# Kernel tuning notes

Measured on AMD Instinct MI355X. Metric: run time of the kernel, lower is better.

Reference implementation:

```python
import jax, jax.numpy as jnp
import numpy as np

B, T, D = 2, 128, 1024
H, R, Dk, Dv = 8, 8, 64, 64


def setup_inputs() -> dict:
    key = jax.random.key(0)
    ks = jax.random.split(key, 11)
    w = lambda k, shp: jax.random.normal(k, shp, dtype=jnp.float32) * 0.02
    return {
        "hidden_states": jax.random.normal(ks[0], (B, T, D), dtype=jnp.float32),
        "Wq": w(ks[1], (D, H * Dk)),
        "Wk": w(ks[2], (D, H * Dk)),
        "Wv": w(ks[3], (D, H * Dv)),
        "Wb": w(ks[4], (D, H * R)),
        "Wtg": w(ks[5], (D, H * R)),
        "mode_logits": jax.random.normal(ks[6], (H, R), dtype=jnp.float32) * 0.1,
        "log_decay": jax.random.normal(ks[7], (H, R), dtype=jnp.float32) * 0.1,
        "omega_log_scale": jax.random.normal(ks[8], (H, R), dtype=jnp.float32) * 0.1,
        "Wg": w(ks[9], (D, H * Dv)),
        "Wo": w(ks[10], (H * Dv, D)),
    }


def _forward(x, Wq, Wk, Wv, Wb, Wtg, mode_logits, log_decay, omega_log_scale, Wg, Wo):
    b, t, _ = x.shape
    # projections
    q = (x @ Wq).reshape(b, t, H, Dk)
    k = (x @ Wk).reshape(b, t, H, Dk)
    v = (x @ Wv).reshape(b, t, H, Dv)
    beta = jax.nn.sigmoid((x @ Wb).reshape(b, t, H, R))
    tg = jax.nn.sigmoid((x @ Wtg).reshape(b, t, H, R))
    # spectral mode parameters
    pair_idx = jnp.arange(0, Dk, 2, dtype=jnp.float32)
    inv_freq = 1.0 / (10000.0 ** (pair_idx / Dk))            # [Dk/2]
    omega = jnp.exp(omega_log_scale)[..., None] * inv_freq    # [H,R,Dk/2]
    omega_full = jnp.repeat(omega, 2, axis=-1)                # [H,R,Dk] (repeat_interleave)
    cos_w = jnp.cos(omega_full)[None, :, :, None, :]          # [1,H,R,1,Dk]
    sin_w = jnp.sin(omega_full)[None, :, :, None, :]
    rho = jnp.exp(-jax.nn.softplus(log_decay))                # [H,R]
    mode_w = jax.nn.softmax(mode_logits, axis=-1)             # [H,R]

    # time-major for scan
    qT = jnp.moveaxis(q, 1, 0)
    kT = jnp.moveaxis(k, 1, 0)
    vT = jnp.moveaxis(v, 1, 0)
    betaT = jnp.moveaxis(beta, 1, 0)
    tgT = jnp.moveaxis(tg, 1, 0)

    def step(carry, xs):
        sr, si = carry                      # [B,H,R,Dv,Dk] each
        q_t, k_t, v_t, b_t, g_t = xs
        decay = (g_t * rho)[..., None, None]            # [B,H,R,1,1]
        rot_r = decay * (cos_w * sr - sin_w * si)
        rot_i = decay * (sin_w * sr + cos_w * si)
        pred = jnp.einsum('bhrvk,bhk->bhrv', rot_r, k_t)
        err = v_t[:, :, None, :] - pred                  # [B,H,R,Dv]
        write = err[..., None] * k_t[:, :, None, None, :]
        sr_new = rot_r + b_t[..., None, None] * write
        read = jnp.einsum('bhrvk,bhk->bhrv', sr_new, q_t)
        y = jnp.einsum('bhrv,hr->bhv', read, mode_w)     # [B,H,Dv]
        return (sr_new, rot_i), y

    s0 = jnp.zeros((b, H, R, Dv, Dk), dtype=x.dtype)
    _, ys = jax.lax.scan(step, (s0, s0), (qT, kT, vT, betaT, tgT))
    o = jnp.moveaxis(ys, 0, 1)                           # [B,T,H,Dv]
    gate = jax.nn.sigmoid((x @ Wg).reshape(b, t, H, Dv))
    o = (o * gate).reshape(b, t, H * Dv)
    return o @ Wo


def reference(hidden_states, Wq, Wk, Wv, Wb, Wtg, mode_logits, log_decay,
              omega_log_scale, Wg, Wo):
    return _forward(hidden_states, Wq, Wk, Wv, Wb, Wtg, mode_logits,
                    log_decay, omega_log_scale, Wg, Wo)
```

## Files before the change

kernel.cpp:

```cpp
#include <hip/hip_runtime.h>
#include <math.h>

#define T_ 128
#define NPROJ 2176
#define CH 32

typedef __attribute__((ext_vector_type(8))) short short8;
typedef __attribute__((ext_vector_type(4))) float float4v;
typedef __attribute__((ext_vector_type(2))) float float2v;

__device__ __forceinline__ ushort f2bf(float x) {
    unsigned u = __float_as_uint(x);
    u += 0x7FFF + ((u >> 16) & 1);
    return (ushort)(u >> 16);
}
__device__ __forceinline__ unsigned pack_bf(float a, float b) {
    unsigned ua = (__float_as_uint(a) + 0x8000u) >> 16;
    unsigned ub = (__float_as_uint(b) + 0x8000u) & 0xffff0000u;
    return ua | ub;
}
__device__ __forceinline__ float bf_lo(unsigned w) { return __uint_as_float(w << 16); }
__device__ __forceinline__ float bf_hi(unsigned w) { return __uint_as_float(w & 0xffff0000u); }

template<int CTRL>
__device__ __forceinline__ float dpp_add(float x) {
    int xi = __float_as_int(x);
    int yi = __builtin_amdgcn_update_dpp(xi, xi, CTRL, 0xF, 0xF, false);
    return x + __int_as_float(yi);
}

__global__ __launch_bounds__(256) void prep_kernel(
    const float* __restrict__ x,
    const float* __restrict__ Wq, const float* __restrict__ Wk,
    const float* __restrict__ Wv, const float* __restrict__ Wb,
    const float* __restrict__ Wtg, const float* __restrict__ Wg,
    const float* __restrict__ Wo,
    const float* __restrict__ mode_logits, const float* __restrict__ log_decay,
    const float* __restrict__ ols,
    float* __restrict__ cosw, float* __restrict__ sinw,
    float* __restrict__ rho, float* __restrict__ modew,
    ushort* __restrict__ xb, ushort* __restrict__ wtb, ushort* __restrict__ wotb,
    float* __restrict__ Acomb)
{
    __shared__ ushort tile[64][68];
    const int blk = blockIdx.x, tid = threadIdx.x;
    if (blk < 16) {
        int idx = blk * 256 + tid;
        if (idx >= 64 * 64) return;
        int t = idx >> 6;
        int k = idx & 63;
        int h = t >> 3;
        if (k == 0) {
            float ld = log_decay[t];
            rho[t] = 1.0f / (1.0f + expf(ld));
            float m = -1e30f;
            for (int i = 0; i < 8; i++) m = fmaxf(m, mode_logits[h * 8 + i]);
            float sum = 0.0f;
            for (int i = 0; i < 8; i++) sum += expf(mode_logits[h * 8 + i] - m);
            modew[t] = expf(mode_logits[t] - m) / sum;
        }
        float osc = expf(ols[t]);
        int p = k >> 1;
        float invf = expf(-((float)(2 * p) / 64.0f) * logf(10000.0f));
        float w = osc * invf;
        cosw[idx] = cosf(w);
        sinw[idx] = sinf(w);
        return;
    }
    if (blk < 80) {
        int base = (blk - 16) * 4096 + tid * 16;
        float4 f0 = *(const float4*)&x[base];
        float4 f1 = *(const float4*)&x[base + 4];
        float4 f2 = *(const float4*)&x[base + 8];
        float4 f3 = *(const float4*)&x[base + 12];
        short8 o0, o1;
        o0[0]=f2bf(f0.x); o0[1]=f2bf(f0.y); o0[2]=f2bf(f0.z); o0[3]=f2bf(f0.w);
        o0[4]=f2bf(f1.x); o0[5]=f2bf(f1.y); o0[6]=f2bf(f1.z); o0[7]=f2bf(f1.w);
        o1[0]=f2bf(f2.x); o1[1]=f2bf(f2.y); o1[2]=f2bf(f2.z); o1[3]=f2bf(f2.w);
        o1[4]=f2bf(f3.x); o1[5]=f2bf(f3.y); o1[6]=f2bf(f3.z); o1[7]=f2bf(f3.w);
        *(short8*)&xb[base] = o0;
        *(short8*)&xb[base + 8] = o1;
        return;
    }
    if (blk >= 752) {
        int base = (blk - 752) * 4096 + tid * 16;
        float4 z = make_float4(0.f, 0.f, 0.f, 0.f);
        *(float4*)&Acomb[base] = z;
        *(float4*)&Acomb[base + 4] = z;
        *(float4*)&Acomb[base + 8] = z;
        *(float4*)&Acomb[base + 12] = z;
        return;
    }
    const float* src; int ld, c0, n0, k0, ldd; ushort* dst;
    if (blk < 624) {
        int b3 = blk - 80; int nt = b3 >> 4, kt = b3 & 15;
        n0 = nt * 64; k0 = kt * 64;
        if (n0 < 512)       { src = Wq;  c0 = n0;        ld = 512; }
        else if (n0 < 1024) { src = Wk;  c0 = n0 - 512;  ld = 512; }
        else if (n0 < 1536) { src = Wv;  c0 = n0 - 1024; ld = 512; }
        else if (n0 < 1600) { src = Wb;  c0 = n0 - 1536; ld = 64;  }
        else if (n0 < 1664) { src = Wtg; c0 = n0 - 1600; ld = 64;  }
        else                { src = Wg;  c0 = n0 - 1664; ld = 512; }
        dst = wtb; ldd = 1024;
    } else {
        int b4 = blk - 624; int nt = b4 >> 3, kt = b4 & 7;
        n0 = nt * 64; k0 = kt * 64;
        src = Wo; c0 = n0; ld = 1024; dst = wotb; ldd = 512;
    }
    #pragma unroll
    for (int rep = 0; rep < 4; rep++) {
        int k = rep * 16 + (tid >> 4);
        int nc = (tid & 15) * 4;
        float4 f = *(const float4*)&src[(size_t)(k0 + k) * ld + c0 + nc];
        tile[nc + 0][k] = f2bf(f.x);
        tile[nc + 1][k] = f2bf(f.y);
        tile[nc + 2][k] = f2bf(f.z);
        tile[nc + 3][k] = f2bf(f.w);
    }
    __syncthreads();
    #pragma unroll
    for (int rep = 0; rep < 4; rep++) {
        int n = rep * 16 + (tid >> 4);
        int kc = (tid & 15) * 4;
        uint2 uu = *(const uint2*)&tile[n][kc];
        *(uint2*)&dst[(size_t)(n0 + n) * ldd + k0 + kc] = uu;
    }
}

__global__ __launch_bounds__(256, 2) void proj_mfma(const ushort* __restrict__ Ab,
        const ushort* __restrict__ BTb, const float* __restrict__ rho,
        float* __restrict__ proj)
{
    __shared__ ushort sA[2][64][40];
    __shared__ ushort sB[2][64][40];
    const int n0 = blockIdx.x * 64, m0 = blockIdx.y * 64;
    const int tid = threadIdx.x;
    const int lane = tid & 63, w = tid >> 6;
    const int wm = w & 1, wn = w >> 1;
    const int l16 = lane & 15, quad = lane >> 4;
    const int srow = tid >> 2, skq = (tid & 3) * 8;
    const ushort* Ag = Ab + (size_t)(m0 + srow) * 1024 + skq;
    const ushort* Bg = BTb + (size_t)(n0 + srow) * 1024 + skq;
    short8 raA = *(const short8*)Ag;
    short8 rbA = *(const short8*)Bg;
    short8 raB = *(const short8*)(Ag + 32);
    short8 rbB = *(const short8*)(Bg + 32);
    float4v acc00 = {0,0,0,0}, acc01 = {0,0,0,0}, acc10 = {0,0,0,0}, acc11 = {0,0,0,0};
    for (int kt = 0; kt < 32; kt += 2) {
        *(short8*)&sA[0][srow][skq] = raA;
        *(short8*)&sB[0][srow][skq] = rbA;
        __syncthreads();
        if (kt + 2 < 32) {
            raA = *(const short8*)(Ag + (kt + 2) * 32);
            rbA = *(const short8*)(Bg + (kt + 2) * 32);
        }
        {
            short8 a0 = *(const short8*)&sA[0][wm * 32 + l16][quad * 8];
            short8 a1 = *(const short8*)&sA[0][wm * 32 + 16 + l16][quad * 8];
            short8 b0 = *(const short8*)&sB[0][wn * 32 + l16][quad * 8];
            short8 b1 = *(const short8*)&sB[0][wn * 32 + 16 + l16][quad * 8];
            acc00 = __builtin_amdgcn_mfma_f32_16x16x32_bf16(a0, b0, acc00, 0, 0, 0);
            acc01 = __builtin_amdgcn_mfma_f32_16x16x32_bf16(a0, b1, acc01, 0, 0, 0);
            acc10 = __builtin_amdgcn_mfma_f32_16x16x32_bf16(a1, b0, acc10, 0, 0, 0);
            acc11 = __builtin_amdgcn_mfma_f32_16x16x32_bf16(a1, b1, acc11, 0, 0, 0);
        }
        *(short8*)&sA[1][srow][skq] = raB;
        *(short8*)&sB[1][srow][skq] = rbB;
        __syncthreads();
        if (kt + 3 < 32) {
            raB = *(const short8*)(Ag + (kt + 3) * 32);
            rbB = *(const short8*)(Bg + (kt + 3) * 32);
        }
        {
            short8 a0 = *(const short8*)&sA[1][wm * 32 + l16][quad * 8];
            short8 a1 = *(const short8*)&sA[1][wm * 32 + 16 + l16][quad * 8];
            short8 b0 = *(const short8*)&sB[1][wn * 32 + l16][quad * 8];
            short8 b1 = *(const short8*)&sB[1][wn * 32 + 16 + l16][quad * 8];
            acc00 = __builtin_amdgcn_mfma_f32_16x16x32_bf16(a0, b0, acc00, 0, 0, 0);
            acc01 = __builtin_amdgcn_mfma_f32_16x16x32_bf16(a0, b1, acc01, 0, 0, 0);
            acc10 = __builtin_amdgcn_mfma_f32_16x16x32_bf16(a1, b0, acc10, 0, 0, 0);
            acc11 = __builtin_amdgcn_mfma_f32_16x16x32_bf16(a1, b1, acc11, 0, 0, 0);
        }
    }
    const bool sig = (n0 >= 1536);
    float m0c = 1.0f, m1c = 1.0f;
    if (n0 == 1600) {
        m0c = rho[wn * 32 + l16];
        m1c = rho[wn * 32 + l16 + 16];
    }
    const int colb = n0 + wn * 32 + l16;
    const int rowb = m0 + wm * 32 + quad * 4;
    #pragma unroll
    for (int r2 = 0; r2 < 4; r2++) {
        float v00 = acc00[r2], v01 = acc01[r2], v10 = acc10[r2], v11 = acc11[r2];
        if (sig) {
            v00 = m0c / (1.0f + expf(-v00));
            v01 = m1c / (1.0f + expf(-v01));
            v10 = m0c / (1.0f + expf(-v10));
            v11 = m1c / (1.0f + expf(-v11));
        }
        proj[(size_t)(rowb + r2) * NPROJ + colb] = v00;
        proj[(size_t)(rowb + r2) * NPROJ + colb + 16] = v01;
        proj[(size_t)(rowb + 16 + r2) * NPROJ + colb] = v10;
        proj[(size_t)(rowb + 16 + r2) * NPROJ + colb + 16] = v11;
    }
}

__global__ __launch_bounds__(256, 2) void scan_kernel(const float* __restrict__ proj,
        const float* __restrict__ cosw, const float* __restrict__ sinw,
        const float* __restrict__ modew, float* __restrict__ Acomb)
{
    __shared__ uint2 qks[2][CH][16][2];
    __shared__ float2 vg[2][CH][16];
    __shared__ float sc4[2][CH][4];
    __shared__ float obuf[CH][16];

    const int bi = blockIdx.x;
    const int s  = bi & 3;
    const int hr = (bi >> 2) & 63;
    const int b  = bi >> 8;
    const int h = hr >> 3, r = hr & 7;
    const int tid = threadIdx.x;
    const int vl = tid >> 4;
    const int kl = tid & 15;

    float2v cw0, cw1, sw0, sw1;
    cw0.x = cosw[hr * 64 + kl * 4 + 0]; cw0.y = cosw[hr * 64 + kl * 4 + 1];
    cw1.x = cosw[hr * 64 + kl * 4 + 2]; cw1.y = cosw[hr * 64 + kl * 4 + 3];
    sw0.x = sinw[hr * 64 + kl * 4 + 0]; sw0.y = sinw[hr * 64 + kl * 4 + 1];
    sw1.x = sinw[hr * 64 + kl * 4 + 2]; sw1.y = sinw[hr * 64 + kl * 4 + 3];
    const float mw = modew[hr];
    float2v sr0 = {0,0}, sr1 = {0,0}, si0 = {0,0}, si1 = {0,0};

    const float* pb = proj + (size_t)b * T_ * NPROJ;
    const int qbase = h * 64;
    const int kbase = 512 + h * 64;
    const int vbase = 1024 + h * 64 + s * 16;
    const int gbase = 1664 + h * 64 + s * 16;
    const int boff  = 1536 + h * 8 + r;
    const int goff  = 1600 + h * 8 + r;

    {
        #pragma unroll
        for (int rep = 0; rep < 4; rep++) {
            int idx = rep * 256 + tid;
            int t = idx >> 5, sub = idx & 31;
            const float* row = pb + (size_t)t * NPROJ;
            float4 f = *(const float4*)(row + (sub < 16 ? qbase + sub * 4
                                                        : kbase + (sub - 16) * 4));
            uint2 pk2; pk2.x = pack_bf(f.x, f.y); pk2.y = pack_bf(f.z, f.w);
            qks[0][t][sub & 15][sub < 16 ? 1 : 0] = pk2;
        }
        #pragma unroll
        for (int rep = 0; rep < 2; rep++) {
            int idx = rep * 256 + tid;
            int t = idx >> 4, v2 = idx & 15;
            const float* row = pb + (size_t)t * NPROJ;
            vg[0][t][v2] = make_float2(row[vbase + v2], row[gbase + v2]);
        }
        if (tid < CH)            sc4[0][tid][0]      = pb[(size_t)tid * NPROJ + boff];
        else if (tid < 2 * CH)   sc4[0][tid - CH][1] = pb[(size_t)(tid - CH) * NPROJ + goff];
    }
    __syncthreads();

    float* dstb = Acomb + ((size_t)b * 128) * 512 + h * 64 + s * 16;

    for (int c = 0; c < T_ / CH; c++) {
        const int cb = c & 1, nb = cb ^ 1;
        const bool have = (c + 1 < T_ / CH);

        float4 g_qk[4]; float2 g_vg[2]; float g_sc = 0.0f;
        if (have) {
            const int t0 = (c + 1) * CH;
            #pragma unroll
            for (int rep = 0; rep < 4; rep++) {
                int idx = rep * 256 + tid;
                int t = idx >> 5, sub = idx & 31;
                const float* row = pb + (size_t)(t0 + t) * NPROJ;
                g_qk[rep] = *(const float4*)(row + (sub < 16 ? qbase + sub * 4
                                                             : kbase + (sub - 16) * 4));
            }
            #pragma unroll
            for (int rep = 0; rep < 2; rep++) {
                int idx = rep * 256 + tid;
                int t = idx >> 4, v2 = idx & 15;
                const float* row = pb + (size_t)(t0 + t) * NPROJ;
                g_vg[rep] = make_float2(row[vbase + v2], row[gbase + v2]);
            }
            if (tid < CH)          g_sc = pb[(size_t)(t0 + tid) * NPROJ + boff];
            else if (tid < 2 * CH) g_sc = pb[(size_t)(t0 + tid - CH) * NPROJ + goff];
        }

        {
            int t = tid >> 3, j = tid & 7;
            uint4 wa = *(const uint4*)&qks[cb][t][2 * j][0];
            uint4 wb = *(const uint4*)&qks[cb][t][2 * j + 1][0];
            float p = bf_lo(wa.x) * bf_lo(wa.z) + bf_hi(wa.x) * bf_hi(wa.z)
                    + bf_lo(wa.y) * bf_lo(wa.w) + bf_hi(wa.y) * bf_hi(wa.w)
                    + bf_lo(wb.x) * bf_lo(wb.z) + bf_hi(wb.x) * bf_hi(wb.z)
                    + bf_lo(wb.y) * bf_lo(wb.w) + bf_hi(wb.y) * bf_hi(wb.w);
            p = dpp_add<0xB1>(p);
            p = dpp_add<0x4E>(p);
            p = dpp_add<0x141>(p);
            if (j == 0) sc4[cb][t][2] = p;
        }
        if (c > 0) {
            #pragma unroll
            for (int rep = 0; rep < 2; rep++) {
                int idx = rep * 256 + tid;
                int t = idx >> 4, v2 = idx & 15;
                atomicAdd(dstb + (size_t)((c - 1) * CH + t) * 512 + v2, obuf[t][v2]);
            }
        }
        __syncthreads();

        const float2* vgb = &vg[cb][0][0];
        const float4* svb = (const float4*)&sc4[cb][0][0];

        uint4 w = *(const uint4*)&qks[cb][0][kl][0];
        float4 sv = svb[0];
        float2 vgv = vgb[vl];
        #pragma unroll
        for (int t = 0; t < CH; t++) {
            uint4 w_n; float4 sv_n; float2 vg_n;
            if (t + 1 < CH) {
                w_n = *(const uint4*)&qks[cb][t + 1][kl][0];
                sv_n = svb[t + 1];
                vg_n = vgb[(t + 1) * 16 + vl];
            }

            float2v k0; k0.x = bf_lo(w.x); k0.y = bf_hi(w.x);
            float2v k1; k1.x = bf_lo(w.y); k1.y = bf_hi(w.y);
            float2v q0; q0.x = bf_lo(w.z); q0.y = bf_hi(w.z);
            float2v q1; q1.x = bf_lo(w.w); q1.y = bf_hi(w.w);

            const float decay = sv.y;
            float2v t1 = cw0 * sr0 - sw0 * si0;
            float2v u1 = sw0 * sr0 + cw0 * si0;
            float2v t2 = cw1 * sr1 - sw1 * si1;
            float2v u2 = sw1 * sr1 + cw1 * si1;
            float2v d2; d2.x = decay; d2.y = decay;
            float2v rr0 = d2 * t1, rr1 = d2 * t2;
            si0 = d2 * u1; si1 = d2 * u2;

            float2v pk2 = rr0 * k0 + rr1 * k1;
            float2v pq2 = rr0 * q0 + rr1 * q1;
            float pk = pk2.x + pk2.y;
            float pq = pq2.x + pq2.y;
            pk = dpp_add<0xB1>(pk);  pq = dpp_add<0xB1>(pq);
            pk = dpp_add<0x4E>(pk);  pq = dpp_add<0x4E>(pq);
            pk = dpp_add<0x141>(pk); pq = dpp_add<0x141>(pq);
            pk = dpp_add<0x140>(pk); pq = dpp_add<0x140>(pq);

            const float sc = sv.x * (vgv.x - pk);
            float2v sc2; sc2.x = sc; sc2.y = sc;
            sr0 = rr0 + sc2 * k0;
            sr1 = rr1 + sc2 * k1;
            const float rp = pq + sc * sv.z;
            if (kl == 0) obuf[t][vl] = mw * rp * vgv.y;

            w = w_n; sv = sv_n; vgv = vg_n;
        }

        if (have) {
            #pragma unroll
            for (int rep = 0; rep < 4; rep++) {
                int idx = rep * 256 + tid;
                int t = idx >> 5, sub = idx & 31;
                float4 f = g_qk[rep];
                uint2 pk2; pk2.x = pack_bf(f.x, f.y); pk2.y = pack_bf(f.z, f.w);
                qks[nb][t][sub & 15][sub < 16 ? 1 : 0] = pk2;
            }
            #pragma unroll
            for (int rep = 0; rep < 2; rep++) {
                int idx = rep * 256 + tid;
                int t = idx >> 4, v2 = idx & 15;
                vg[nb][t][v2] = g_vg[rep];
            }
            if (tid < CH)          sc4[nb][tid][0]      = g_sc;
            else if (tid < 2 * CH) sc4[nb][tid - CH][1] = g_sc;
        }
        __syncthreads();
    }
    #pragma unroll
    for (int rep = 0; rep < 2; rep++) {
        int idx = rep * 256 + tid;
        int t = idx >> 4, v2 = idx & 15;
        atomicAdd(dstb + (size_t)(3 * CH + t) * 512 + v2, obuf[t][v2]);
    }
}

__global__ __launch_bounds__(256, 2) void out_mfma(const float* __restrict__ Af,
        const ushort* __restrict__ BTb, float* __restrict__ C)
{
    __shared__ ushort sA[2][64][40];
    __shared__ ushort sB[2][64][40];
    const int n0 = blockIdx.x * 64, m0 = blockIdx.y * 64;
    const int tid = threadIdx.x;
    const int lane = tid & 63, w = tid >> 6;
    const int wm = w & 1, wn = w >> 1;
    const int l16 = lane & 15, quad = lane >> 4;
    const int srow = tid >> 2, skq = (tid & 3) * 8;
    const float* Ag = Af + (size_t)(m0 + srow) * 512 + skq;
    const ushort* Bg = BTb + (size_t)(n0 + srow) * 512 + skq;
    float4 fa0A = *(const float4*)Ag;
    float4 fa1A = *(const float4*)(Ag + 4);
    short8 rbA  = *(const short8*)Bg;
    float4 fa0B = *(const float4*)(Ag + 32);
    float4 fa1B = *(const float4*)(Ag + 36);
    short8 rbB  = *(const short8*)(Bg + 32);
    float4v acc00 = {0,0,0,0}, acc01 = {0,0,0,0}, acc10 = {0,0,0,0}, acc11 = {0,0,0,0};
    for (int kt = 0; kt < 16; kt += 2) {
        {
            short8 ra;
            ra[0]=f2bf(fa0A.x); ra[1]=f2bf(fa0A.y); ra[2]=f2bf(fa0A.z); ra[3]=f2bf(fa0A.w);
            ra[4]=f2bf(fa1A.x); ra[5]=f2bf(fa1A.y); ra[6]=f2bf(fa1A.z); ra[7]=f2bf(fa1A.w);
            *(short8*)&sA[0][srow][skq] = ra;
            *(short8*)&sB[0][srow][skq] = rbA;
        }
        __syncthreads();
        if (kt + 2 < 16) {
            fa0A = *(const float4*)(Ag + (kt + 2) * 32);
            fa1A = *(const float4*)(Ag + (kt + 2) * 32 + 4);
            rbA  = *(const short8*)(Bg + (kt + 2) * 32);
        }
        {
            short8 a0 = *(const short8*)&sA[0][wm * 32 + l16][quad * 8];
            short8 a1 = *(const short8*)&sA[0][wm * 32 + 16 + l16][quad * 8];
            short8 b0 = *(const short8*)&sB[0][wn * 32 + l16][quad * 8];
            short8 b1 = *(const short8*)&sB[0][wn * 32 + 16 + l16][quad * 8];
            acc00 = __builtin_amdgcn_mfma_f32_16x16x32_bf16(a0, b0, acc00, 0, 0, 0);
            acc01 = __builtin_amdgcn_mfma_f32_16x16x32_bf16(a0, b1, acc01, 0, 0, 0);
            acc10 = __builtin_amdgcn_mfma_f32_16x16x32_bf16(a1, b0, acc10, 0, 0, 0);
            acc11 = __builtin_amdgcn_mfma_f32_16x16x32_bf16(a1, b1, acc11, 0, 0, 0);
        }
        {
            short8 ra;
            ra[0]=f2bf(fa0B.x); ra[1]=f2bf(fa0B.y); ra[2]=f2bf(fa0B.z); ra[3]=f2bf(fa0B.w);
            ra[4]=f2bf(fa1B.x); ra[5]=f2bf(fa1B.y); ra[6]=f2bf(fa1B.z); ra[7]=f2bf(fa1B.w);
            *(short8*)&sA[1][srow][skq] = ra;
            *(short8*)&sB[1][srow][skq] = rbB;
        }
        __syncthreads();
        if (kt + 3 < 16) {
            fa0B = *(const float4*)(Ag + (kt + 3) * 32);
            fa1B = *(const float4*)(Ag + (kt + 3) * 32 + 4);
            rbB  = *(const short8*)(Bg + (kt + 3) * 32);
        }
        {
            short8 a0 = *(const short8*)&sA[1][wm * 32 + l16][quad * 8];
            short8 a1 = *(const short8*)&sA[1][wm * 32 + 16 + l16][quad * 8];
            short8 b0 = *(const short8*)&sB[1][wn * 32 + l16][quad * 8];
            short8 b1 = *(const short8*)&sB[1][wn * 32 + 16 + l16][quad * 8];
            acc00 = __builtin_amdgcn_mfma_f32_16x16x32_bf16(a0, b0, acc00, 0, 0, 0);
            acc01 = __builtin_amdgcn_mfma_f32_16x16x32_bf16(a0, b1, acc01, 0, 0, 0);
            acc10 = __builtin_amdgcn_mfma_f32_16x16x32_bf16(a1, b0, acc10, 0, 0, 0);
            acc11 = __builtin_amdgcn_mfma_f32_16x16x32_bf16(a1, b1, acc11, 0, 0, 0);
        }
    }
    const int colb = n0 + wn * 32 + l16;
    const int rowb = m0 + wm * 32 + quad * 4;
    #pragma unroll
    for (int r2 = 0; r2 < 4; r2++) {
        C[(size_t)(rowb + r2) * 1024 + colb] = acc00[r2];
        C[(size_t)(rowb + r2) * 1024 + colb + 16] = acc01[r2];
        C[(size_t)(rowb + 16 + r2) * 1024 + colb] = acc10[r2];
        C[(size_t)(rowb + 16 + r2) * 1024 + colb + 16] = acc11[r2];
    }
}

extern "C" void kernel_launch(void* const* d_in, const int* in_sizes, int n_in,
                              void* d_out, int out_size, void* d_ws, size_t ws_size,
                              hipStream_t stream) {
    const float* x   = (const float*)d_in[0];
    const float* Wq  = (const float*)d_in[1];
    const float* Wk  = (const float*)d_in[2];
    const float* Wv  = (const float*)d_in[3];
    const float* Wb  = (const float*)d_in[4];
    const float* Wtg = (const float*)d_in[5];
    const float* ml  = (const float*)d_in[6];
    const float* ldc = (const float*)d_in[7];
    const float* ols = (const float*)d_in[8];
    const float* Wg  = (const float*)d_in[9];
    const float* Wo  = (const float*)d_in[10];
    float* out = (float*)d_out;

    float* ws = (float*)d_ws;
    float* proj    = ws;
    float* cosw    = proj + 256 * NPROJ;
    float* sinw    = cosw + 4096;
    float* rho     = sinw + 4096;
    float* modew   = rho + 64;
    ushort* xb     = (ushort*)(modew + 64);
    ushort* wotb   = (ushort*)((float*)xb + 131072);
    float*  Acomb  = (float*)wotb + 262144;
    ushort* wtb    = (ushort*)(Acomb + 131072);

    prep_kernel<<<784, 256, 0, stream>>>(x, Wq, Wk, Wv, Wb, Wtg, Wg, Wo,
                                         ml, ldc, ols, cosw, sinw, rho, modew,
                                         xb, wtb, wotb, Acomb);
    proj_mfma<<<dim3(34, 4), 256, 0, stream>>>(xb, wtb, rho, proj);
    scan_kernel<<<512, 256, 0, stream>>>(proj, cosw, sinw, modew, Acomb);
    out_mfma<<<dim3(16, 4), 256, 0, stream>>>(Acomb, wotb, out);
}
```

Measured before the change: 135.1 us.

## Split scan state across 512 threads with two k-elements each

The scan kernel now launches 512 threads per block. Each thread holds 2 k-dimension elements of the state instead of 4, and the dot-product reductions gain a ds_swizzle step so they span 32 lanes. The decay multiply is moved out of the reduction chain and applied to the reduced scalars afterwards, which shortens the serial dependency inside each time step. The q/k shared-memory layout and the staging loads are reorganised to match. The aim is to cut per-step latency in the sequential recurrence, at the cost of an extra cross-lane shuffle, more threads per block and possible occupancy pressure.

```diff
diff --git a/kernel.cpp b/kernel.cpp
--- a/kernel.cpp
+++ b/kernel.cpp
@@ -26,6 +26,10 @@
 __device__ __forceinline__ float dpp_add(float x) {
     int xi = __float_as_int(x);
     int yi = __builtin_amdgcn_update_dpp(xi, xi, CTRL, 0xF, 0xF, false);
+    return x + __int_as_float(yi);
+}
+__device__ __forceinline__ float swz_add16(float x) {
+    int yi = __builtin_amdgcn_ds_swizzle(__float_as_int(x), 0x401F);
     return x + __int_as_float(yi);
 }
 
@@ -206,11 +210,11 @@
     }
 }
 
-__global__ __launch_bounds__(256, 2) void scan_kernel(const float* __restrict__ proj,
+__global__ __launch_bounds__(512, 4) void scan_kernel(const float* __restrict__ proj,
         const float* __restrict__ cosw, const float* __restrict__ sinw,
         const float* __restrict__ modew, float* __restrict__ Acomb)
 {
-    __shared__ uint2 qks[2][CH][16][2];
+    __shared__ unsigned qks[2][CH][64];
     __shared__ float2 vg[2][CH][16];
     __shared__ float sc4[2][CH][4];
     __shared__ float obuf[CH][16];
@@ -221,16 +225,14 @@
     const int b  = bi >> 8;
     const int h = hr >> 3, r = hr & 7;
     const int tid = threadIdx.x;
-    const int vl = tid >> 4;
-    const int kl = tid & 15;
-
-    float2v cw0, cw1, sw0, sw1;
-    cw0.x = cosw[hr * 64 + kl * 4 + 0]; cw0.y = cosw[hr * 64 + kl * 4 + 1];
-    cw1.x = cosw[hr * 64 + kl * 4 + 2]; cw1.y = cosw[hr * 64 + kl * 4 + 3];
-    sw0.x = sinw[hr * 64 + kl * 4 + 0]; sw0.y = sinw[hr * 64 + kl * 4 + 1];
-    sw1.x = sinw[hr * 64 + kl * 4 + 2]; sw1.y = sinw[hr * 64 + kl * 4 + 3];
+    const int vl = tid >> 5;
+    const int kl = tid & 31;
+
+    float2v cw0, sw0;
+    cw0.x = cosw[hr * 64 + kl * 2 + 0]; cw0.y = cosw[hr * 64 + kl * 2 + 1];
+    sw0.x = sinw[hr * 64 + kl * 2 + 0]; sw0.y = sinw[hr * 64 + kl * 2 + 1];
     const float mw = modew[hr];
-    float2v sr0 = {0,0}, sr1 = {0,0}, si0 = {0,0}, si1 = {0,0};
+    float2v sr0 = {0,0}, si0 = {0,0};
 
     const float* pb = proj + (size_t)b * T_ * NPROJ;
     const int qbase = h * 64;
@@ -242,19 +244,17 @@
 
     {
         #pragma unroll
-        for (int rep = 0; rep < 4; rep++) {
-            int idx = rep * 256 + tid;
+        for (int rep = 0; rep < 2; rep++) {
+            int idx = rep * 512 + tid;
             int t = idx >> 5, sub = idx & 31;
             const float* row = pb + (size_t)t * NPROJ;
-            float4 f = *(const float4*)(row + (sub < 16 ? qbase + sub * 4
-                                                        : kbase + (sub - 16) * 4));
+            float4 f = *(const float4*)(row + (sub < 16 ? kbase + sub * 4
+                                                        : qbase + (sub - 16) * 4));
             uint2 pk2; pk2.x = pack_bf(f.x, f.y); pk2.y = pack_bf(f.z, f.w);
-            qks[0][t][sub & 15][sub < 16 ? 1 : 0] = pk2;
-        }
-        #pragma unroll
-        for (int rep = 0; rep < 2; rep++) {
-            int idx = rep * 256 + tid;
-            int t = idx >> 4, v2 = idx & 15;
+            *(uint2*)&qks[0][t][sub < 16 ? 2 * sub : 32 + 2 * (sub - 16)] = pk2;
+        }
+        {
+            int t = tid >> 4, v2 = tid & 15;
             const float* row = pb + (size_t)t * NPROJ;
             vg[0][t][v2] = make_float2(row[vbase + v2], row[gbase + v2]);
         }
@@ -269,123 +269,122 @@
         const int cb = c & 1, nb = cb ^ 1;
         const bool have = (c + 1 < T_ / CH);
 
-        float4 g_qk[4]; float2 g_vg[2]; float g_sc = 0.0f;
+        float4 g_qk0, g_qk1; float2 g_vg0; float g_sc = 0.0f;
         if (have) {
             const int t0 = (c + 1) * CH;
-            #pragma unroll
-            for (int rep = 0; rep < 4; rep++) {
-                int idx = rep * 256 + tid;
+            {
+                int idx = tid;
                 int t = idx >> 5, sub = idx & 31;
                 const float* row = pb + (size_t)(t0 + t) * NPROJ;
-                g_qk[rep] = *(const float4*)(row + (sub < 16 ? qbase + sub * 4
-                                                             : kbase + (sub - 16) * 4));
-            }
-            #pragma unroll
-            for (int rep = 0; rep < 2; rep++) {
-                int idx = rep * 256 + tid;
-                int t = idx >> 4, v2 = idx & 15;
+                g_qk0 = *(const float4*)(row + (sub < 16 ? kbase + sub * 4
+                                                         : qbase + (sub - 16) * 4));
+            }
+            {
+                int idx = 512 + tid;
+                int t = idx >> 5, sub = idx & 31;
                 const float* row = pb + (size_t)(t0 + t) * NPROJ;
-                g_vg[rep] = make_float2(row[vbase + v2], row[gbase + v2]);
+                g_qk1 = *(const float4*)(row + (sub < 16 ? kbase + sub * 4
+                                                         : qbase + (sub - 16) * 4));
+            }
+            {
+                int t = tid >> 4, v2 = tid & 15;
+                const float* row = pb + (size_t)(t0 + t) * NPROJ;
+                g_vg0 = make_float2(row[vbase + v2], row[gbase + v2]);
             }
             if (tid < CH)          g_sc = pb[(size_t)(t0 + tid) * NPROJ + boff];
             else if (tid < 2 * CH) g_sc = pb[(size_t)(t0 + tid - CH) * NPROJ + goff];
         }
 
         {
-            int t = tid >> 3, j = tid & 7;
-            uint4 wa = *(const uint4*)&qks[cb][t][2 * j][0];
-            uint4 wb = *(const uint4*)&qks[cb][t][2 * j + 1][0];
-            float p = bf_lo(wa.x) * bf_lo(wa.z) + bf_hi(wa.x) * bf_hi(wa.z)
-                    + bf_lo(wa.y) * bf_lo(wa.w) + bf_hi(wa.y) * bf_hi(wa.w)
-                    + bf_lo(wb.x) * bf_lo(wb.z) + bf_hi(wb.x) * bf_hi(wb.z)
-                    + bf_lo(wb.y) * bf_lo(wb.w) + bf_hi(wb.y) * bf_hi(wb.w);
+            int t = tid >> 4, j = tid & 15;
+            uint2 kk = *(const uint2*)&qks[cb][t][2 * j];
+            uint2 qq = *(const uint2*)&qks[cb][t][32 + 2 * j];
+            float p = bf_lo(kk.x) * bf_lo(qq.x) + bf_hi(kk.x) * bf_hi(qq.x)
+                    + bf_lo(kk.y) * bf_lo(qq.y) + bf_hi(kk.y) * bf_hi(qq.y);
             p = dpp_add<0xB1>(p);
             p = dpp_add<0x4E>(p);
             p = dpp_add<0x141>(p);
+            p = dpp_add<0x140>(p);
             if (j == 0) sc4[cb][t][2] = p;
         }
         if (c > 0) {
-            #pragma unroll
-            for (int rep = 0; rep < 2; rep++) {
-                int idx = rep * 256 + tid;
-                int t = idx >> 4, v2 = idx & 15;
-                atomicAdd(dstb + (size_t)((c - 1) * CH + t) * 512 + v2, obuf[t][v2]);
-            }
+            int t = tid >> 4, v2 = tid & 15;
+            atomicAdd(dstb + (size_t)((c - 1) * CH + t) * 512 + v2, obuf[t][v2]);
         }
         __syncthreads();
 
         const float2* vgb = &vg[cb][0][0];
         const float4* svb = (const float4*)&sc4[cb][0][0];
-
-        uint4 w = *(const uint4*)&qks[cb][0][kl][0];
+        const unsigned* qd_base = &qks[cb][0][0];
+
+        unsigned kd = qd_base[kl];
+        unsigned qd = qd_base[32 + kl];
         float4 sv = svb[0];
         float2 vgv = vgb[vl];
         #pragma unroll
         for (int t = 0; t < CH; t++) {
-            uint4 w_n; float4 sv_n; float2 vg_n;
+            unsigned kd_n, qd_n; float4 sv_n; float2 vg_n;
             if (t + 1 < CH) {
-                w_n = *(const uint4*)&qks[cb][t + 1][kl][0];
+                kd_n = qd_base[(t + 1) * 64 + kl];
+                qd_n = qd_base[(t + 1) * 64 + 32 + kl];
                 sv_n = svb[t + 1];
                 vg_n = vgb[(t + 1) * 16 + vl];
             }
 
-            float2v k0; k0.x = bf_lo(w.x); k0.y = bf_hi(w.x);
-            float2v k1; k1.x = bf_lo(w.y); k1.y = bf_hi(w.y);
-            float2v q0; q0.x = bf_lo(w.z); q0.y = bf_hi(w.z);
-            float2v q1; q1.x = bf_lo(w.w); q1.y = bf_hi(w.w);
+            float2v k0; k0.x = bf_lo(kd); k0.y = bf_hi(kd);
+            float2v q0; q0.x = bf_lo(qd); q0.y = bf_hi(qd);
 
             const float decay = sv.y;
             float2v t1 = cw0 * sr0 - sw0 * si0;
             float2v u1 = sw0 * sr0 + cw0 * si0;
-            float2v t2 = cw1 * sr1 - sw1 * si1;
-            float2v u2 = sw1 * sr1 + cw1 * si1;
-            float2v d2; d2.x = decay; d2.y = decay;
-            float2v rr0 = d2 * t1, rr1 = d2 * t2;
-            si0 = d2 * u1; si1 = d2 * u2;
-
-            float2v pk2 = rr0 * k0 + rr1 * k1;
-            float2v pq2 = rr0 * q0 + rr1 * q1;
+            float2v pk2 = t1 * k0;
+            float2v pq2 = t1 * q0;
             float pk = pk2.x + pk2.y;
             float pq = pq2.x + pq2.y;
             pk = dpp_add<0xB1>(pk);  pq = dpp_add<0xB1>(pq);
             pk = dpp_add<0x4E>(pk);  pq = dpp_add<0x4E>(pq);
             pk = dpp_add<0x141>(pk); pq = dpp_add<0x141>(pq);
             pk = dpp_add<0x140>(pk); pq = dpp_add<0x140>(pq);
-
-            const float sc = sv.x * (vgv.x - pk);
+            pk = swz_add16(pk);      pq = swz_add16(pq);
+
+            float2v d2; d2.x = decay; d2.y = decay;
+            float2v rr0 = d2 * t1;
+            si0 = d2 * u1;
+            const float bd = sv.x * decay;
+            const float bv = sv.x * vgv.x;
+            const float sc = bv - bd * pk;
             float2v sc2; sc2.x = sc; sc2.y = sc;
             sr0 = rr0 + sc2 * k0;
-            sr1 = rr1 + sc2 * k1;
-            const float rp = pq + sc * sv.z;
+            const float rp = decay * pq + sc * sv.z;
             if (kl == 0) obuf[t][vl] = mw * rp * vgv.y;
 
-            w = w_n; sv = sv_n; vgv = vg_n;
+            kd = kd_n; qd = qd_n; sv = sv_n; vgv = vg_n;
         }
 
         if (have) {
-            #pragma unroll
-            for (int rep = 0; rep < 4; rep++) {
-                int idx = rep * 256 + tid;
+            {
+                int idx = tid;
                 int t = idx >> 5, sub = idx & 31;
-                float4 f = g_qk[rep];
-                uint2 pk2; pk2.x = pack_bf(f.x, f.y); pk2.y = pack_bf(f.z, f.w);
-                qks[nb][t][sub & 15][sub < 16 ? 1 : 0] = pk2;
-            }
-            #pragma unroll
-            for (int rep = 0; rep < 2; rep++) {
-                int idx = rep * 256 + tid;
-                int t = idx >> 4, v2 = idx & 15;
-                vg[nb][t][v2] = g_vg[rep];
+                uint2 pk2; pk2.x = pack_bf(g_qk0.x, g_qk0.y); pk2.y = pack_bf(g_qk0.z, g_qk0.w);
+                *(uint2*)&qks[nb][t][sub < 16 ? 2 * sub : 32 + 2 * (sub - 16)] = pk2;
+            }
+            {
+                int idx = 512 + tid;
+                int t = idx >> 5, sub = idx & 31;
+                uint2 pk2; pk2.x = pack_bf(g_qk1.x, g_qk1.y); pk2.y = pack_bf(g_qk1.z, g_qk1.w);
+                *(uint2*)&qks[nb][t][sub < 16 ? 2 * sub : 32 + 2 * (sub - 16)] = pk2;
+            }
+            {
+                int t = tid >> 4, v2 = tid & 15;
+                vg[nb][t][v2] = g_vg0;
             }
             if (tid < CH)          sc4[nb][tid][0]      = g_sc;
             else if (tid < 2 * CH) sc4[nb][tid - CH][1] = g_sc;
         }
         __syncthreads();
     }
-    #pragma unroll
-    for (int rep = 0; rep < 2; rep++) {
-        int idx = rep * 256 + tid;
-        int t = idx >> 4, v2 = idx & 15;
+    {
+        int t = tid >> 4, v2 = tid & 15;
         atomicAdd(dstb + (size_t)(3 * CH + t) * 512 + v2, obuf[t][v2]);
     }
 }
@@ -500,6 +499,6 @@
                                          ml, ldc, ols, cosw, sinw, rho, modew,
                                          xb, wtb, wotb, Acomb);
     proj_mfma<<<dim3(34, 4), 256, 0, stream>>>(xb, wtb, rho, proj);
-    scan_kernel<<<512, 256, 0, stream>>>(proj, cosw, sinw, modew, Acomb);
+    scan_kernel<<<512, 512, 0, stream>>>(proj, cosw, sinw, modew, Acomb);
     out_mfma<<<dim3(16, 4), 256, 0, stream>>>(Acomb, wotb, out);
 }
```

New measurement: 151.9 us. +12.4%, slower.
